# Optimization experiments

Hardware: AMD Instinct MI355X
Metric: run time of the kernel (lower is better)

## Reference

```python
import jax, jax.numpy as jnp
from jax import lax
import numpy as np

LEVELS = 5
KSIZE = 45
SIGMA0 = 1.0
SIZE_ADDER = 0
SIGMA_MULT = 2.0


def _gauss1d(ksize, sigma):
    # Matches cv2.getGaussianKernel for sigma > 0: normalized Gaussian samples.
    x = np.arange(ksize, dtype=np.float64) - (ksize - 1) / 2.0
    g = np.exp(-(x * x) / (2.0 * sigma * sigma))
    return g / g.sum()


def _gauss2d(ksize, sigma):
    g1 = _gauss1d(ksize, sigma)
    return jnp.asarray(np.outer(g1, g1), dtype=jnp.float32)  # (k, k)


_KERNELS = [_gauss2d(KSIZE + SIZE_ADDER, SIGMA0 * SIGMA_MULT ** lvl) for lvl in range(LEVELS)]


def _blur(img, k2d):
    """Depthwise 2D Gaussian blur with replicate padding. img: (N,C,H,W), k2d: (k,k)."""
    C = img.shape[1]
    k = k2d.shape[0]
    pad = k // 2
    imgp = jnp.pad(img, ((0, 0), (0, 0), (pad, pad), (pad, pad)), mode='edge')
    kern = jnp.broadcast_to(k2d.astype(img.dtype), (C, 1, k, k))  # same filter per channel
    return lax.conv_general_dilated(
        imgp, kern, window_strides=(1, 1), padding='VALID',
        dimension_numbers=('NCHW', 'OIHW', 'NCHW'), feature_group_count=C)


def _blend(img0, img1, mask):
    # Fused Laplacian-stack build for img0/img1, Gaussian-stack for mask, and
    # lerp + sum-over-levels accumulation in a single pass over levels.
    cur0, cur1, curm = img0, img1, mask
    acc = jnp.zeros_like(img0)
    for lvl in range(LEVELS):
        if lvl < LEVELS - 1:
            k2d = _KERNELS[lvl]
            b0 = _blur(cur0, k2d)
            b1 = _blur(cur1, k2d)
            bm = _blur(curm, k2d)
            lap0 = cur0 - b0
            lap1 = cur1 - b1
            acc = acc + lap0 + curm * (lap1 - lap0)  # lerp(lap0, lap1, gauss_mask)
            cur0, cur1, curm = b0, b1, bm
        else:
            acc = acc + cur0 + curm * (cur1 - cur0)
    return acc


def setup_inputs() -> dict:
    key = jax.random.key(0)
    k0, k1, k2 = jax.random.split(key, 3)
    img0 = jax.random.normal(k0, (16, 3, 512, 512), dtype=jnp.float32)
    img1 = jax.random.normal(k1, (16, 3, 512, 512), dtype=jnp.float32)
    mask = jax.random.uniform(k2, (16, 1, 512, 512), dtype=jnp.float32)
    return {"img0": img0, "img1": img1, "mask": mask}


def reference(img0, img1, mask):
    return _blend(img0, img1, mask)
```

## Files before the change

### kernel.cpp

```cpp
#include <hip/hip_runtime.h>

#define PH 512
#define PW 512
#define PLANE (PH * PW)

enum { M_F0 = 0, M_MID = 1, M_MONLY = 2, M_LAST = 3 };

constexpr double cexp_pos(double z) {
  double term = 1.0, sum = 1.0;
  for (int k = 1; k < 160; ++k) {
    term *= z / (double)k;
    sum += term;
  }
  return sum;
}
template <int LVL, int R>
struct WTab {
  float w[2 * R + 1];
  constexpr WTab() : w{} {
    double sig = 1.0;
    for (int i = 0; i < LVL; ++i) sig *= 2.0;
    double g[2 * R + 1] = {};
    double s = 0.0;
    for (int t = 0; t <= 2 * R; ++t) {
      double x = (double)(t - R);
      g[t] = 1.0 / cexp_pos((x * x) / (2.0 * sig * sig));
      s += g[t];
    }
    for (int t = 0; t <= 2 * R; ++t) w[t] = (float)(g[t] / s);
  }
};

__device__ __forceinline__ int clampi(int v, int hi) {
  return v < 0 ? 0 : (v > hi ? hi : v);
}
__device__ __forceinline__ int swz(int bid, int nwg) {
  const int q = nwg >> 3;
  return (bid & 7) * q + (bid >> 3);
}
union HU { ushort u; _Float16 h; };
union BU { uint4 q; ushort u[8]; };
__device__ __forceinline__ float h2f(ushort s) {
  HU x; x.u = s; return (float)x.h;
}
__device__ __forceinline__ ushort f2h(float f) {
  HU x; x.h = (_Float16)f; return x.u;
}
__device__ __forceinline__ void q2f8(uint4 q, float* v) {
  BU b; b.q = q;
#pragma unroll
  for (int j = 0; j < 8; ++j) v[j] = h2f(b.u[j]);
}
__device__ __forceinline__ void sth8(ushort* __restrict__ p, const float* v) {
  BU b;
#pragma unroll
  for (int j = 0; j < 8; ++j) b.u[j] = f2h(v[j]);
  *(uint4*)p = b.q;
}
__device__ __forceinline__ void ff2f8(float4 a, float4 b, float* v) {
  v[0] = a.x; v[1] = a.y; v[2] = a.z; v[3] = a.w;
  v[4] = b.x; v[5] = b.y; v[6] = b.z; v[7] = b.w;
}
__device__ __forceinline__ void stf8(float* __restrict__ p, const float* v) {
  *(float4*)p = make_float4(v[0], v[1], v[2], v[3]);
  *(float4*)(p + 4) = make_float4(v[4], v[5], v[6], v[7]);
}

template <int LVL, int R, int MODE>
__global__ __launch_bounds__(512) void fused_lvl(
    const ushort* __restrict__ Sc, const ushort* __restrict__ Smk,
    const ushort* __restrict__ Gm4p, const float* __restrict__ in0,
    const float* __restrict__ in1, const float* __restrict__ inm,
    ushort* __restrict__ oS, ushort* __restrict__ oM,
    ushort* __restrict__ accP, float* __restrict__ outp, int cn3) {
  constexpr WTab<LVL, R> WT;
  constexpr int R8 = ((R + 7) / 8) * 8;
  constexpr int WW = 64 + 2 * R8;
  constexpr int WSTR = WW + 6;
  constexpr int VWIN = 64 + 2 * R;
  constexpr int NCH = WW / 8;
  constexpr int NJOBS = VWIN * NCH;
  constexpr int NHJ = VWIN * 8;
  __shared__ float Wb[VWIN * WSTR];

  const int bid = swz(blockIdx.x, gridDim.x);
  const int tid = threadIdx.x;
  const int p = bid >> 6, t = bid & 63;
  const int tx = t & 7;
  const int x0 = tx << 6, y0 = (t >> 3) << 6;
  const bool edge = (tx == 0) || (tx == 7);
  const int ey = tid >> 3, exq = (tid & 7) << 3;
  const size_t erow = (size_t)(y0 + ey) * PW + x0 + exq;

  const bool ismask = (MODE == M_MONLY) || (MODE != M_LAST && p >= cn3);
  const int pm = ismask ? ((MODE == M_MONLY) ? p : p - cn3) : 0;
  const int n = p / 3;

  uint4 qacc{}, qm{}, qm4{};
  float4 fi0a{}, fi0b{}, fmka{}, fmkb{};
  if (!ismask) {
    if (MODE == M_F0) {
      const float* p0 = in0 + (size_t)p * PLANE + erow;
      fi0a = ((const float4*)p0)[0];
      fi0b = ((const float4*)p0)[1];
      const float* pk = inm + (size_t)n * PLANE + erow;
      fmka = ((const float4*)pk)[0];
      fmkb = ((const float4*)pk)[1];
    } else {
      qacc = *(const uint4*)(accP + (size_t)p * PLANE + erow);
      qm = *(const uint4*)(Smk + (size_t)n * PLANE + erow);
      if (MODE == M_LAST)
        qm4 = *(const uint4*)(Gm4p + (size_t)n * PLANE + erow);
    }
  }

  for (int j0 = tid; j0 < NJOBS; j0 += 512) {
    const int row = j0 / NCH, ch = j0 % NCH;
    const int gy = clampi(y0 + row - R, PH - 1);
    const int gx = x0 - R8 + (ch << 3);
    float v[8];
    if (MODE == M_F0) {
      if (!ismask) {
        const float* r0 = in0 + (size_t)p * PLANE + (size_t)gy * PW;
        const float* r1 = in1 + (size_t)p * PLANE + (size_t)gy * PW;
        if (!edge || (gx >= 0 && gx <= PW - 8)) {
          float a[8], bb[8];
          ff2f8(((const float4*)(r0 + gx))[0], ((const float4*)(r0 + gx))[1], a);
          ff2f8(((const float4*)(r1 + gx))[0], ((const float4*)(r1 + gx))[1], bb);
#pragma unroll
          for (int j = 0; j < 8; ++j) v[j] = bb[j] - a[j];
        } else {
#pragma unroll
          for (int j = 0; j < 8; ++j) {
            const int cx = clampi(gx + j, PW - 1);
            v[j] = r1[cx] - r0[cx];
          }
        }
      } else {
        const float* rm = inm + (size_t)pm * PLANE + (size_t)gy * PW;
        if (!edge || (gx >= 0 && gx <= PW - 8)) {
          ff2f8(((const float4*)(rm + gx))[0], ((const float4*)(rm + gx))[1], v);
        } else {
#pragma unroll
          for (int j = 0; j < 8; ++j) v[j] = rm[clampi(gx + j, PW - 1)];
        }
      }
    } else {
      const ushort* sp =
          (ismask ? Smk + (size_t)pm * PLANE : Sc + (size_t)p * PLANE) +
          (size_t)gy * PW;
      if (!edge || (gx >= 0 && gx <= PW - 8)) {
        q2f8(*(const uint4*)&sp[gx], v);
      } else {
#pragma unroll
        for (int j = 0; j < 8; ++j) v[j] = h2f(sp[clampi(gx + j, PW - 1)]);
      }
    }
    float* d = &Wb[row * WSTR + (ch << 3)];
#pragma unroll
    for (int k = 0; k < 4; ++k)
      *(float2*)&d[2 * k] = make_float2(v[2 * k], v[2 * k + 1]);
  }
  __syncthreads();

  float D[8];
  if (!ismask) {
    const float* dp = &Wb[(R + ey) * WSTR + R8 + exq];
#pragma unroll
    for (int k = 0; k < 4; ++k) {
      const float2 dv = *(const float2*)(dp + 2 * k);
      D[2 * k] = dv.x;
      D[2 * k + 1] = dv.y;
    }
  }
  __syncthreads();

  for (int j0 = tid; j0 < NHJ; j0 += 512) {
    const int r = j0 >> 3, cg = j0 & 7;
    constexpr int basep = R8 - R;
    const float* wr = &Wb[r * WSTR + basep + (cg << 3)];
    float a[8];
#pragma unroll
    for (int i = 0; i < 8; ++i) a[i] = 0.f;
#pragma unroll
    for (int j2 = 0; j2 < R + 4; ++j2) {
      const float2 v2 = *(const float2*)&wr[2 * j2];
      const int j0e = 2 * j2, j1e = 2 * j2 + 1;
#pragma unroll
      for (int i = 0; i < 8; ++i) {
        if (i <= j0e && j0e - i <= 2 * R) a[i] = fmaf(WT.w[j0e - i], v2.x, a[i]);
        if (i <= j1e && j1e - i <= 2 * R) a[i] = fmaf(WT.w[j1e - i], v2.y, a[i]);
      }
    }
    float* hr = &Wb[r * WSTR + (cg << 3)];
#pragma unroll
    for (int k = 0; k < 4; ++k)
      *(float2*)&hr[2 * k] = make_float2(a[2 * k], a[2 * k + 1]);
  }
  __syncthreads();

  const int lane = tid & 63, yg = tid >> 6;
  float b[8];
#pragma unroll
  for (int i = 0; i < 8; ++i) b[i] = 0.f;
#pragma unroll
  for (int j = 0; j < 2 * R + 8; ++j) {
    const float v = Wb[((yg << 3) + j) * WSTR + lane];
#pragma unroll
    for (int i = 0; i < 8; ++i)
      if (i <= j && j - i <= 2 * R) b[i] = fmaf(WT.w[j - i], v, b[i]);
  }
  __syncthreads();

#pragma unroll
  for (int i = 0; i < 8; ++i) Wb[lane * 65 + (yg << 3) + i] = b[i];
  __syncthreads();
  float bs[8];
#pragma unroll
  for (int j = 0; j < 8; ++j) bs[j] = Wb[(exq + j) * 65 + ey];

  if (ismask) {
    sth8(oM + (size_t)pm * PLANE + erow, bs);
    return;
  }

  if (MODE == M_F0) {
    float i0v[8], mv[8], av[8];
    ff2f8(fi0a, fi0b, i0v);
    ff2f8(fmka, fmkb, mv);
#pragma unroll
    for (int j = 0; j < 8; ++j) av[j] = i0v[j] + mv[j] * (D[j] - bs[j]);
    sth8(accP + (size_t)p * PLANE + erow, av);
    sth8(oS + (size_t)p * PLANE + erow, bs);
  } else if (MODE == M_MID) {
    float av[8], mv[8];
    q2f8(qacc, av);
    q2f8(qm, mv);
#pragma unroll
    for (int j = 0; j < 8; ++j) av[j] += mv[j] * (D[j] - bs[j]);
    sth8(accP + (size_t)p * PLANE + erow, av);
    sth8(oS + (size_t)p * PLANE + erow, bs);
  } else {
    float av[8], m3[8], m4[8], o[8];
    q2f8(qacc, av);
    q2f8(qm, m3);
    q2f8(qm4, m4);
#pragma unroll
    for (int j = 0; j < 8; ++j)
      o[j] = av[j] + m3[j] * (D[j] - bs[j]) + m4[j] * bs[j];
    stf8(outp + (size_t)p * PLANE + erow, o);
  }
}

extern "C" void kernel_launch(void* const* d_in, const int* in_sizes, int n_in,
                              void* d_out, int out_size, void* d_ws,
                              size_t ws_size, hipStream_t stream) {
  const float* img0 = (const float*)d_in[0];
  const float* img1 = (const float*)d_in[1];
  const float* mask = (const float*)d_in[2];
  float* out = (float*)d_out;

  const int NTOT = 16;
  const size_t perImg = (size_t)11 * PLANE * sizeof(ushort);
  int CN = 16;
  while (CN > 1 && (size_t)CN * perImg > ws_size) CN >>= 1;

  for (int s = 0; s < NTOT; s += CN) {
    ushort* SA = (ushort*)d_ws;
    ushort* SB = SA + (size_t)4 * CN * PLANE;
    ushort* acc = SB + (size_t)4 * CN * PLANE;
    ushort* SAm = SA + (size_t)3 * CN * PLANE;
    ushort* SBm = SB + (size_t)3 * CN * PLANE;

    const float* in0 = img0 + (size_t)s * 3 * PLANE;
    const float* in1 = img1 + (size_t)s * 3 * PLANE;
    const float* inm = mask + (size_t)s * PLANE;
    float* o = out + (size_t)s * 3 * PLANE;

    const int cn3 = 3 * CN;
    const dim3 blk(512);
    const int gAll = 4 * CN * 64, gD = 3 * CN * 64, gM = CN * 64;
    const ushort* nb = nullptr;
    const float* nf = nullptr;

    hipLaunchKernelGGL((fused_lvl<0, 6, M_F0>), dim3(gAll), blk, 0, stream, nb,
                       nb, nb, in0, in1, inm, SA, SAm, acc, (float*)nullptr,
                       cn3);
    hipLaunchKernelGGL((fused_lvl<1, 10, M_MID>), dim3(gAll), blk, 0, stream,
                       SA, SAm, nb, nf, nf, nf, SB, SBm, acc, (float*)nullptr,
                       cn3);
    hipLaunchKernelGGL((fused_lvl<2, 18, M_MID>), dim3(gAll), blk, 0, stream,
                       SB, SBm, nb, nf, nf, nf, SA, SAm, acc, (float*)nullptr,
                       cn3);
    hipLaunchKernelGGL((fused_lvl<3, 22, M_MONLY>), dim3(gM), blk, 0, stream,
                       nb, SAm, nb, nf, nf, nf, (ushort*)nullptr, SBm,
                       (ushort*)nullptr, (float*)nullptr, cn3);
    hipLaunchKernelGGL((fused_lvl<3, 22, M_LAST>), dim3(gD), blk, 0, stream, SA,
                       SAm, SBm, nf, nf, nf, (ushort*)nullptr,
                       (ushort*)nullptr, acc, o, cn3);
  }
}
```

Baseline: 216.5 us.

## Process K tiles per block with register prefetch of next tile window

New measurement: 258.2 us. 19.3% more time.

```diff
diff --git a/kernel.cpp b/kernel.cpp
--- a/kernel.cpp
+++ b/kernel.cpp
@@ -66,7 +66,7 @@
   *(float4*)(p + 4) = make_float4(v[4], v[5], v[6], v[7]);
 }
 
-template <int LVL, int R, int MODE>
+template <int LVL, int R, int MODE, int K>
 __global__ __launch_bounds__(512) void fused_lvl(
     const ushort* __restrict__ Sc, const ushort* __restrict__ Smk,
     const ushort* __restrict__ Gm4p, const float* __restrict__ in0,
@@ -80,175 +80,230 @@
   constexpr int VWIN = 64 + 2 * R;
   constexpr int NCH = WW / 8;
   constexpr int NJOBS = VWIN * NCH;
+  constexpr int JPT = (NJOBS + 511) / 512;
   constexpr int NHJ = VWIN * 8;
   __shared__ float Wb[VWIN * WSTR];
 
   const int bid = swz(blockIdx.x, gridDim.x);
   const int tid = threadIdx.x;
-  const int p = bid >> 6, t = bid & 63;
-  const int tx = t & 7;
-  const int x0 = tx << 6, y0 = (t >> 3) << 6;
-  const bool edge = (tx == 0) || (tx == 7);
+  const int gt0 = bid * K;
+  const int p = gt0 >> 6;
+  const int t0 = gt0 & 63;
   const int ey = tid >> 3, exq = (tid & 7) << 3;
-  const size_t erow = (size_t)(y0 + ey) * PW + x0 + exq;
 
   const bool ismask = (MODE == M_MONLY) || (MODE != M_LAST && p >= cn3);
   const int pm = ismask ? ((MODE == M_MONLY) ? p : p - cn3) : 0;
   const int n = p / 3;
 
-  uint4 qacc{}, qm{}, qm4{};
-  float4 fi0a{}, fi0b{}, fmka{}, fmkb{};
-  if (!ismask) {
+  const float* r0base = (MODE == M_F0 && !ismask) ? in0 + (size_t)p * PLANE : nullptr;
+  const float* r1base = (MODE == M_F0 && !ismask) ? in1 + (size_t)p * PLANE : nullptr;
+  const float* rmbase = (MODE == M_F0 && ismask) ? inm + (size_t)pm * PLANE : nullptr;
+  const ushort* sbase =
+      (MODE != M_F0) ? (ismask ? Smk + (size_t)pm * PLANE : Sc + (size_t)p * PLANE)
+                     : nullptr;
+
+  auto loadWin = [&](int x0, int y0, bool edge, float (&wv)[JPT][8]) {
+#pragma unroll
+    for (int i = 0; i < JPT; ++i) {
+      const int j0 = tid + (i << 9);
+      if (j0 < NJOBS) {
+        const int row = j0 / NCH, ch = j0 % NCH;
+        const int gy = clampi(y0 + row - R, PH - 1);
+        const int gx = x0 - R8 + (ch << 3);
+        if (MODE == M_F0) {
+          if (!ismask) {
+            const float* r0 = r0base + (size_t)gy * PW;
+            const float* r1 = r1base + (size_t)gy * PW;
+            if (!edge || (gx >= 0 && gx <= PW - 8)) {
+              float a[8], bb[8];
+              ff2f8(((const float4*)(r0 + gx))[0], ((const float4*)(r0 + gx))[1], a);
+              ff2f8(((const float4*)(r1 + gx))[0], ((const float4*)(r1 + gx))[1], bb);
+#pragma unroll
+              for (int j = 0; j < 8; ++j) wv[i][j] = bb[j] - a[j];
+            } else {
+#pragma unroll
+              for (int j = 0; j < 8; ++j) {
+                const int cx = clampi(gx + j, PW - 1);
+                wv[i][j] = r1[cx] - r0[cx];
+              }
+            }
+          } else {
+            const float* rm = rmbase + (size_t)gy * PW;
+            if (!edge || (gx >= 0 && gx <= PW - 8)) {
+              ff2f8(((const float4*)(rm + gx))[0], ((const float4*)(rm + gx))[1],
+                    wv[i]);
+            } else {
+#pragma unroll
+              for (int j = 0; j < 8; ++j) wv[i][j] = rm[clampi(gx + j, PW - 1)];
+            }
+          }
+        } else {
+          const ushort* sp = sbase + (size_t)gy * PW;
+          if (!edge || (gx >= 0 && gx <= PW - 8)) {
+            q2f8(*(const uint4*)&sp[gx], wv[i]);
+          } else {
+#pragma unroll
+            for (int j = 0; j < 8; ++j) wv[i][j] = h2f(sp[clampi(gx + j, PW - 1)]);
+          }
+        }
+      }
+    }
+  };
+  auto writeWin = [&](const float (&wv)[JPT][8]) {
+#pragma unroll
+    for (int i = 0; i < JPT; ++i) {
+      const int j0 = tid + (i << 9);
+      if (j0 < NJOBS) {
+        const int row = j0 / NCH, ch = j0 % NCH;
+        float* d = &Wb[row * WSTR + (ch << 3)];
+#pragma unroll
+        for (int k2 = 0; k2 < 4; ++k2)
+          *(float2*)&d[2 * k2] = make_float2(wv[i][2 * k2], wv[i][2 * k2 + 1]);
+      }
+    }
+  };
+  struct Epi { float4 fa, fb, fc, fd; uint4 qa, qb, qc; };
+  auto loadEpi = [&](size_t erow, Epi& e) {
+    if (ismask) return;
     if (MODE == M_F0) {
       const float* p0 = in0 + (size_t)p * PLANE + erow;
-      fi0a = ((const float4*)p0)[0];
-      fi0b = ((const float4*)p0)[1];
+      e.fa = ((const float4*)p0)[0];
+      e.fb = ((const float4*)p0)[1];
       const float* pk = inm + (size_t)n * PLANE + erow;
-      fmka = ((const float4*)pk)[0];
-      fmkb = ((const float4*)pk)[1];
+      e.fc = ((const float4*)pk)[0];
+      e.fd = ((const float4*)pk)[1];
     } else {
-      qacc = *(const uint4*)(accP + (size_t)p * PLANE + erow);
-      qm = *(const uint4*)(Smk + (size_t)n * PLANE + erow);
-      if (MODE == M_LAST)
-        qm4 = *(const uint4*)(Gm4p + (size_t)n * PLANE + erow);
-    }
-  }
-
-  for (int j0 = tid; j0 < NJOBS; j0 += 512) {
-    const int row = j0 / NCH, ch = j0 % NCH;
-    const int gy = clampi(y0 + row - R, PH - 1);
-    const int gx = x0 - R8 + (ch << 3);
-    float v[8];
-    if (MODE == M_F0) {
-      if (!ismask) {
-        const float* r0 = in0 + (size_t)p * PLANE + (size_t)gy * PW;
-        const float* r1 = in1 + (size_t)p * PLANE + (size_t)gy * PW;
-        if (!edge || (gx >= 0 && gx <= PW - 8)) {
-          float a[8], bb[8];
-          ff2f8(((const float4*)(r0 + gx))[0], ((const float4*)(r0 + gx))[1], a);
-          ff2f8(((const float4*)(r1 + gx))[0], ((const float4*)(r1 + gx))[1], bb);
-#pragma unroll
-          for (int j = 0; j < 8; ++j) v[j] = bb[j] - a[j];
-        } else {
-#pragma unroll
-          for (int j = 0; j < 8; ++j) {
-            const int cx = clampi(gx + j, PW - 1);
-            v[j] = r1[cx] - r0[cx];
+      e.qa = *(const uint4*)(accP + (size_t)p * PLANE + erow);
+      e.qb = *(const uint4*)(Smk + (size_t)n * PLANE + erow);
+      if (MODE == M_LAST) e.qc = *(const uint4*)(Gm4p + (size_t)n * PLANE + erow);
+    }
+  };
+
+  float wvA[JPT][8], wvB[JPT][8];
+  Epi eA{}, eB{};
+  {
+    const int t = t0;
+    const int x0 = (t & 7) << 6, y0 = (t >> 3) << 6;
+    const bool edge = ((t & 7) == 0) || ((t & 7) == 7);
+    loadWin(x0, y0, edge, wvA);
+    loadEpi((size_t)(y0 + ey) * PW + x0 + exq, eA);
+  }
+
+#pragma unroll
+  for (int k = 0; k < K; ++k) {
+    const int t = t0 + k;
+    const int tx = t & 7;
+    const int x0 = tx << 6, y0 = (t >> 3) << 6;
+    const size_t erow = (size_t)(y0 + ey) * PW + x0 + exq;
+
+    __syncthreads();
+    writeWin(wvA);
+    if (k + 1 < K) {
+      const int tn = t0 + k + 1;
+      const int xn = (tn & 7) << 6, yn = (tn >> 3) << 6;
+      const bool edn = ((tn & 7) == 0) || ((tn & 7) == 7);
+      loadWin(xn, yn, edn, wvB);
+      loadEpi((size_t)(yn + ey) * PW + xn + exq, eB);
+    }
+    __syncthreads();
+
+    float D[8];
+    if (!ismask) {
+      const float* dp = &Wb[(R + ey) * WSTR + R8 + exq];
+#pragma unroll
+      for (int k2 = 0; k2 < 4; ++k2) {
+        const float2 dv = *(const float2*)(dp + 2 * k2);
+        D[2 * k2] = dv.x;
+        D[2 * k2 + 1] = dv.y;
+      }
+    }
+    __syncthreads();
+
+#pragma unroll
+    for (int i = 0; i < (NHJ + 511) / 512; ++i) {
+      const int j0 = tid + (i << 9);
+      if (j0 < NHJ) {
+        const int r = j0 >> 3, cg = j0 & 7;
+        constexpr int basep = R8 - R;
+        const float* wr = &Wb[r * WSTR + basep + (cg << 3)];
+        float a[8];
+#pragma unroll
+        for (int i2 = 0; i2 < 8; ++i2) a[i2] = 0.f;
+#pragma unroll
+        for (int j2 = 0; j2 < R + 4; ++j2) {
+          const float2 v2 = *(const float2*)&wr[2 * j2];
+          const int j0e = 2 * j2, j1e = 2 * j2 + 1;
+#pragma unroll
+          for (int i2 = 0; i2 < 8; ++i2) {
+            if (i2 <= j0e && j0e - i2 <= 2 * R)
+              a[i2] = fmaf(WT.w[j0e - i2], v2.x, a[i2]);
+            if (i2 <= j1e && j1e - i2 <= 2 * R)
+              a[i2] = fmaf(WT.w[j1e - i2], v2.y, a[i2]);
           }
         }
-      } else {
-        const float* rm = inm + (size_t)pm * PLANE + (size_t)gy * PW;
-        if (!edge || (gx >= 0 && gx <= PW - 8)) {
-          ff2f8(((const float4*)(rm + gx))[0], ((const float4*)(rm + gx))[1], v);
-        } else {
-#pragma unroll
-          for (int j = 0; j < 8; ++j) v[j] = rm[clampi(gx + j, PW - 1)];
-        }
+        float* hr = &Wb[r * WSTR + (cg << 3)];
+#pragma unroll
+        for (int k2 = 0; k2 < 4; ++k2)
+          *(float2*)&hr[2 * k2] = make_float2(a[2 * k2], a[2 * k2 + 1]);
       }
+    }
+    __syncthreads();
+
+    const int lane = tid & 63, yg = tid >> 6;
+    float b[8];
+#pragma unroll
+    for (int i = 0; i < 8; ++i) b[i] = 0.f;
+#pragma unroll
+    for (int j = 0; j < 2 * R + 8; ++j) {
+      const float v = Wb[((yg << 3) + j) * WSTR + lane];
+#pragma unroll
+      for (int i = 0; i < 8; ++i)
+        if (i <= j && j - i <= 2 * R) b[i] = fmaf(WT.w[j - i], v, b[i]);
+    }
+    __syncthreads();
+#pragma unroll
+    for (int i = 0; i < 8; ++i) Wb[lane * 65 + (yg << 3) + i] = b[i];
+    __syncthreads();
+    float bs[8];
+#pragma unroll
+    for (int j = 0; j < 8; ++j) bs[j] = Wb[(exq + j) * 65 + ey];
+
+    if (ismask) {
+      sth8(oM + (size_t)pm * PLANE + erow, bs);
+    } else if (MODE == M_F0) {
+      float i0v[8], mv[8], av[8];
+      ff2f8(eA.fa, eA.fb, i0v);
+      ff2f8(eA.fc, eA.fd, mv);
+#pragma unroll
+      for (int j = 0; j < 8; ++j) av[j] = i0v[j] + mv[j] * (D[j] - bs[j]);
+      sth8(accP + (size_t)p * PLANE + erow, av);
+      sth8(oS + (size_t)p * PLANE + erow, bs);
+    } else if (MODE == M_MID) {
+      float av[8], mv[8];
+      q2f8(eA.qa, av);
+      q2f8(eA.qb, mv);
+#pragma unroll
+      for (int j = 0; j < 8; ++j) av[j] += mv[j] * (D[j] - bs[j]);
+      sth8(accP + (size_t)p * PLANE + erow, av);
+      sth8(oS + (size_t)p * PLANE + erow, bs);
     } else {
-      const ushort* sp =
-          (ismask ? Smk + (size_t)pm * PLANE : Sc + (size_t)p * PLANE) +
-          (size_t)gy * PW;
-      if (!edge || (gx >= 0 && gx <= PW - 8)) {
-        q2f8(*(const uint4*)&sp[gx], v);
-      } else {
-#pragma unroll
-        for (int j = 0; j < 8; ++j) v[j] = h2f(sp[clampi(gx + j, PW - 1)]);
-      }
-    }
-    float* d = &Wb[row * WSTR + (ch << 3)];
-#pragma unroll
-    for (int k = 0; k < 4; ++k)
-      *(float2*)&d[2 * k] = make_float2(v[2 * k], v[2 * k + 1]);
-  }
-  __syncthreads();
-
-  float D[8];
-  if (!ismask) {
-    const float* dp = &Wb[(R + ey) * WSTR + R8 + exq];
-#pragma unroll
-    for (int k = 0; k < 4; ++k) {
-      const float2 dv = *(const float2*)(dp + 2 * k);
-      D[2 * k] = dv.x;
-      D[2 * k + 1] = dv.y;
-    }
-  }
-  __syncthreads();
-
-  for (int j0 = tid; j0 < NHJ; j0 += 512) {
-    const int r = j0 >> 3, cg = j0 & 7;
-    constexpr int basep = R8 - R;
-    const float* wr = &Wb[r * WSTR + basep + (cg << 3)];
-    float a[8];
-#pragma unroll
-    for (int i = 0; i < 8; ++i) a[i] = 0.f;
-#pragma unroll
-    for (int j2 = 0; j2 < R + 4; ++j2) {
-      const float2 v2 = *(const float2*)&wr[2 * j2];
-      const int j0e = 2 * j2, j1e = 2 * j2 + 1;
-#pragma unroll
-      for (int i = 0; i < 8; ++i) {
-        if (i <= j0e && j0e - i <= 2 * R) a[i] = fmaf(WT.w[j0e - i], v2.x, a[i]);
-        if (i <= j1e && j1e - i <= 2 * R) a[i] = fmaf(WT.w[j1e - i], v2.y, a[i]);
-      }
-    }
-    float* hr = &Wb[r * WSTR + (cg << 3)];
-#pragma unroll
-    for (int k = 0; k < 4; ++k)
-      *(float2*)&hr[2 * k] = make_float2(a[2 * k], a[2 * k + 1]);
-  }
-  __syncthreads();
-
-  const int lane = tid & 63, yg = tid >> 6;
-  float b[8];
-#pragma unroll
-  for (int i = 0; i < 8; ++i) b[i] = 0.f;
-#pragma unroll
-  for (int j = 0; j < 2 * R + 8; ++j) {
-    const float v = Wb[((yg << 3) + j) * WSTR + lane];
-#pragma unroll
-    for (int i = 0; i < 8; ++i)
-      if (i <= j && j - i <= 2 * R) b[i] = fmaf(WT.w[j - i], v, b[i]);
-  }
-  __syncthreads();
-
-#pragma unroll
-  for (int i = 0; i < 8; ++i) Wb[lane * 65 + (yg << 3) + i] = b[i];
-  __syncthreads();
-  float bs[8];
-#pragma unroll
-  for (int j = 0; j < 8; ++j) bs[j] = Wb[(exq + j) * 65 + ey];
-
-  if (ismask) {
-    sth8(oM + (size_t)pm * PLANE + erow, bs);
-    return;
-  }
-
-  if (MODE == M_F0) {
-    float i0v[8], mv[8], av[8];
-    ff2f8(fi0a, fi0b, i0v);
-    ff2f8(fmka, fmkb, mv);
-#pragma unroll
-    for (int j = 0; j < 8; ++j) av[j] = i0v[j] + mv[j] * (D[j] - bs[j]);
-    sth8(accP + (size_t)p * PLANE + erow, av);
-    sth8(oS + (size_t)p * PLANE + erow, bs);
-  } else if (MODE == M_MID) {
-    float av[8], mv[8];
-    q2f8(qacc, av);
-    q2f8(qm, mv);
-#pragma unroll
-    for (int j = 0; j < 8; ++j) av[j] += mv[j] * (D[j] - bs[j]);
-    sth8(accP + (size_t)p * PLANE + erow, av);
-    sth8(oS + (size_t)p * PLANE + erow, bs);
-  } else {
-    float av[8], m3[8], m4[8], o[8];
-    q2f8(qacc, av);
-    q2f8(qm, m3);
-    q2f8(qm4, m4);
-#pragma unroll
-    for (int j = 0; j < 8; ++j)
-      o[j] = av[j] + m3[j] * (D[j] - bs[j]) + m4[j] * bs[j];
-    stf8(outp + (size_t)p * PLANE + erow, o);
+      float av[8], m3[8], m4[8], o[8];
+      q2f8(eA.qa, av);
+      q2f8(eA.qb, m3);
+      q2f8(eA.qc, m4);
+#pragma unroll
+      for (int j = 0; j < 8; ++j)
+        o[j] = av[j] + m3[j] * (D[j] - bs[j]) + m4[j] * bs[j];
+      stf8(outp + (size_t)p * PLANE + erow, o);
+    }
+
+    if (k + 1 < K) {
+#pragma unroll
+      for (int i = 0; i < JPT; ++i)
+#pragma unroll
+        for (int j = 0; j < 8; ++j) wvA[i][j] = wvB[i][j];
+      eA = eB;
+    }
   }
 }
 
@@ -260,6 +315,7 @@
   const float* mask = (const float*)d_in[2];
   float* out = (float*)d_out;
 
+  constexpr int K = 4;
   const int NTOT = 16;
   const size_t perImg = (size_t)11 * PLANE * sizeof(ushort);
   int CN = 16;
@@ -279,24 +335,24 @@
 
     const int cn3 = 3 * CN;
     const dim3 blk(512);
-    const int gAll = 4 * CN * 64, gD = 3 * CN * 64, gM = CN * 64;
+    const int gAll = 4 * CN * 64 / K, gD = 3 * CN * 64 / K, gM = CN * 64 / K;
     const ushort* nb = nullptr;
     const float* nf = nullptr;
 
-    hipLaunchKernelGGL((fused_lvl<0, 6, M_F0>), dim3(gAll), blk, 0, stream, nb,
-                       nb, nb, in0, in1, inm, SA, SAm, acc, (float*)nullptr,
+    hipLaunchKernelGGL((fused_lvl<0, 6, M_F0, K>), dim3(gAll), blk, 0, stream,
+                       nb, nb, nb, in0, in1, inm, SA, SAm, acc, (float*)nullptr,
                        cn3);
-    hipLaunchKernelGGL((fused_lvl<1, 10, M_MID>), dim3(gAll), blk, 0, stream,
+    hipLaunchKernelGGL((fused_lvl<1, 10, M_MID, K>), dim3(gAll), blk, 0, stream,
                        SA, SAm, nb, nf, nf, nf, SB, SBm, acc, (float*)nullptr,
                        cn3);
-    hipLaunchKernelGGL((fused_lvl<2, 18, M_MID>), dim3(gAll), blk, 0, stream,
+    hipLaunchKernelGGL((fused_lvl<2, 18, M_MID, K>), dim3(gAll), blk, 0, stream,
                        SB, SBm, nb, nf, nf, nf, SA, SAm, acc, (float*)nullptr,
                        cn3);
-    hipLaunchKernelGGL((fused_lvl<3, 22, M_MONLY>), dim3(gM), blk, 0, stream,
+    hipLaunchKernelGGL((fused_lvl<3, 22, M_MONLY, K>), dim3(gM), blk, 0, stream,
                        nb, SAm, nb, nf, nf, nf, (ushort*)nullptr, SBm,
                        (ushort*)nullptr, (float*)nullptr, cn3);
-    hipLaunchKernelGGL((fused_lvl<3, 22, M_LAST>), dim3(gD), blk, 0, stream, SA,
-                       SAm, SBm, nf, nf, nf, (ushort*)nullptr,
+    hipLaunchKernelGGL((fused_lvl<3, 22, M_LAST, K>), dim3(gD), blk, 0, stream,
+                       SA, SAm, SBm, nf, nf, nf, (ushort*)nullptr,
                        (ushort*)nullptr, acc, o, cn3);
   }
 }
```

## Remove in-place LDS hazard syncs and fetch center values from global

Applied to the files above, without the earlier changes.

Measured after the change: 245.5 us. 13.4% more time.

```diff
diff --git a/kernel.cpp b/kernel.cpp
--- a/kernel.cpp
+++ b/kernel.cpp
@@ -76,11 +76,12 @@
   constexpr WTab<LVL, R> WT;
   constexpr int R8 = ((R + 7) / 8) * 8;
   constexpr int WW = 64 + 2 * R8;
-  constexpr int WSTR = WW + 6;
+  constexpr int WSTR = WW + 7;
   constexpr int VWIN = 64 + 2 * R;
   constexpr int NCH = WW / 8;
   constexpr int NJOBS = VWIN * NCH;
   constexpr int NHJ = VWIN * 8;
+  constexpr int HITER = (NHJ + 511) / 512;
   __shared__ float Wb[VWIN * WSTR];
 
   const int bid = swz(blockIdx.x, gridDim.x);
@@ -96,19 +97,23 @@
   const int pm = ismask ? ((MODE == M_MONLY) ? p : p - cn3) : 0;
   const int n = p / 3;
 
-  uint4 qacc{}, qm{}, qm4{};
-  float4 fi0a{}, fi0b{}, fmka{}, fmkb{};
+  uint4 qacc{}, qm{}, qm4{}, qd{};
+  float4 fi0a{}, fi0b{}, fi1a{}, fi1b{}, fmka{}, fmkb{};
   if (!ismask) {
     if (MODE == M_F0) {
       const float* p0 = in0 + (size_t)p * PLANE + erow;
       fi0a = ((const float4*)p0)[0];
       fi0b = ((const float4*)p0)[1];
+      const float* p1 = in1 + (size_t)p * PLANE + erow;
+      fi1a = ((const float4*)p1)[0];
+      fi1b = ((const float4*)p1)[1];
       const float* pk = inm + (size_t)n * PLANE + erow;
       fmka = ((const float4*)pk)[0];
       fmkb = ((const float4*)pk)[1];
     } else {
       qacc = *(const uint4*)(accP + (size_t)p * PLANE + erow);
       qm = *(const uint4*)(Smk + (size_t)n * PLANE + erow);
+      qd = *(const uint4*)(Sc + (size_t)p * PLANE + erow);
       if (MODE == M_LAST)
         qm4 = *(const uint4*)(Gm4p + (size_t)n * PLANE + erow);
     }
@@ -158,44 +163,43 @@
     }
     float* d = &Wb[row * WSTR + (ch << 3)];
 #pragma unroll
-    for (int k = 0; k < 4; ++k)
-      *(float2*)&d[2 * k] = make_float2(v[2 * k], v[2 * k + 1]);
-  }
-  __syncthreads();
-
-  float D[8];
-  if (!ismask) {
-    const float* dp = &Wb[(R + ey) * WSTR + R8 + exq];
-#pragma unroll
-    for (int k = 0; k < 4; ++k) {
-      const float2 dv = *(const float2*)(dp + 2 * k);
-      D[2 * k] = dv.x;
-      D[2 * k + 1] = dv.y;
-    }
-  }
-  __syncthreads();
-
-  for (int j0 = tid; j0 < NHJ; j0 += 512) {
-    const int r = j0 >> 3, cg = j0 & 7;
-    constexpr int basep = R8 - R;
-    const float* wr = &Wb[r * WSTR + basep + (cg << 3)];
-    float a[8];
-#pragma unroll
-    for (int i = 0; i < 8; ++i) a[i] = 0.f;
-#pragma unroll
-    for (int j2 = 0; j2 < R + 4; ++j2) {
-      const float2 v2 = *(const float2*)&wr[2 * j2];
-      const int j0e = 2 * j2, j1e = 2 * j2 + 1;
-#pragma unroll
-      for (int i = 0; i < 8; ++i) {
-        if (i <= j0e && j0e - i <= 2 * R) a[i] = fmaf(WT.w[j0e - i], v2.x, a[i]);
-        if (i <= j1e && j1e - i <= 2 * R) a[i] = fmaf(WT.w[j1e - i], v2.y, a[i]);
+    for (int k = 0; k < 8; ++k) d[k] = v[k];
+  }
+  __syncthreads();
+
+  float ha[HITER][8];
+#pragma unroll
+  for (int i = 0; i < HITER; ++i) {
+    const int j0 = tid + (i << 9);
+    if (j0 < NHJ) {
+      const int r = j0 >> 3, cg = j0 & 7;
+      constexpr int basep = R8 - R;
+      const float* wr = &Wb[r * WSTR + basep + (cg << 3)];
+      float a[8];
+#pragma unroll
+      for (int i2 = 0; i2 < 8; ++i2) a[i2] = 0.f;
+#pragma unroll
+      for (int j = 0; j < 2 * R + 8; ++j) {
+        const float v = wr[j];
+#pragma unroll
+        for (int i2 = 0; i2 < 8; ++i2)
+          if (i2 <= j && j - i2 <= 2 * R) a[i2] = fmaf(WT.w[j - i2], v, a[i2]);
       }
-    }
-    float* hr = &Wb[r * WSTR + (cg << 3)];
-#pragma unroll
-    for (int k = 0; k < 4; ++k)
-      *(float2*)&hr[2 * k] = make_float2(a[2 * k], a[2 * k + 1]);
+#pragma unroll
+      for (int k = 0; k < 8; ++k) ha[i][k] = a[k];
+    }
+  }
+  __syncthreads();
+
+#pragma unroll
+  for (int i = 0; i < HITER; ++i) {
+    const int j0 = tid + (i << 9);
+    if (j0 < NHJ) {
+      const int r = j0 >> 3, cg = j0 & 7;
+      float* hr = &Wb[r * WSTR + (cg << 3)];
+#pragma unroll
+      for (int k = 0; k < 8; ++k) hr[k] = ha[i][k];
+    }
   }
   __syncthreads();
 
@@ -225,26 +229,30 @@
   }
 
   if (MODE == M_F0) {
-    float i0v[8], mv[8], av[8];
+    float i0v[8], i1v[8], mv[8], av[8];
     ff2f8(fi0a, fi0b, i0v);
+    ff2f8(fi1a, fi1b, i1v);
     ff2f8(fmka, fmkb, mv);
 #pragma unroll
-    for (int j = 0; j < 8; ++j) av[j] = i0v[j] + mv[j] * (D[j] - bs[j]);
+    for (int j = 0; j < 8; ++j)
+      av[j] = i0v[j] + mv[j] * ((i1v[j] - i0v[j]) - bs[j]);
     sth8(accP + (size_t)p * PLANE + erow, av);
     sth8(oS + (size_t)p * PLANE + erow, bs);
   } else if (MODE == M_MID) {
-    float av[8], mv[8];
+    float av[8], mv[8], D[8];
     q2f8(qacc, av);
     q2f8(qm, mv);
+    q2f8(qd, D);
 #pragma unroll
     for (int j = 0; j < 8; ++j) av[j] += mv[j] * (D[j] - bs[j]);
     sth8(accP + (size_t)p * PLANE + erow, av);
     sth8(oS + (size_t)p * PLANE + erow, bs);
   } else {
-    float av[8], m3[8], m4[8], o[8];
+    float av[8], m3[8], m4[8], D[8], o[8];
     q2f8(qacc, av);
     q2f8(qm, m3);
     q2f8(qm4, m4);
+    q2f8(qd, D);
 #pragma unroll
     for (int j = 0; j < 8; ++j)
       o[j] = av[j] + m3[j] * (D[j] - bs[j]) + m4[j] * bs[j];
```
